# Performance work log

Measured on AMD Instinct MI355X. Metric: run time of the kernel, lower is better.

## Reference

```python
import jax, jax.numpy as jnp
import numpy as np

N_TREE = 200
DEPTH = 3
N_LEAF = 2 ** (DEPTH + 1) - 1      # 15 internal decision nodes
N_LEAVES = N_LEAF + 1              # 16 leaves
N_NODE = 64
BATCH = 2048
D_FEAT = 512
LR = 0.01


def _leaf_paths(depth):
    """For each of the 2^(depth+1) leaves, the internal-node index and the
    left/right bit at every level (matches the tf.gather index construction:
    bit==0 -> take p, bit==1 -> take 1-p; children of node n are 2n+1, 2n+2)."""
    L = 2 ** (depth + 1)
    nodes = np.zeros((L, depth + 1), np.int32)
    bits = np.zeros((L, depth + 1), np.int32)
    for l in range(L):
        node = 0
        for d in range(depth + 1):
            bit = (l >> (depth - d)) & 1
            nodes[l, d] = node
            bits[l, d] = bit
            node = 2 * node + 1 + bit
    return nodes, bits

_NODES, _BITS = _leaf_paths(DEPTH)


def setup_inputs() -> dict:
    key = jax.random.key(0)
    ks = jax.random.split(key, 9)
    u = lambda k, s: jax.random.uniform(k, s, jnp.float32, -0.05, 0.05)  # keras 'uniform' init
    return {
        "x": jax.random.normal(ks[0], (BATCH, D_FEAT), jnp.float32),
        "y_true": jax.random.normal(ks[1], (BATCH, 1), jnp.float32),
        "w_t": u(ks[2], (N_TREE, D_FEAT, N_NODE)),
        "b_t": u(ks[3], (N_TREE, N_NODE)),
        "w_d": u(ks[4], (N_TREE, N_NODE, N_LEAF)),
        "b_d": u(ks[5], (N_TREE, N_LEAF)),
        "w_l": u(ks[6], (N_TREE, N_LEAVES)),
        "b_l": u(ks[7], (N_TREE,)),
        "f_0": jnp.full((1,), 0.5, jnp.float32),
    }


def reference(x, y_true, w_t, b_t, w_d, b_d, w_l, b_l, f_0):
    B = x.shape[0]
    # Batched per-tree small MLP (the 200-iteration Python loop in the original).
    # Dropout is identity at inference.
    h = jax.nn.relu(jnp.einsum('bd,tdn->tbn', x, w_t) + b_t[:, None, :])        # [T,B,N_NODE]
    p = jax.nn.sigmoid(jnp.einsum('tbn,tnl->tbl', h, w_d) + b_d[:, None, :])    # [T,B,15]
    # Soft binary-tree routing: mu[t,b,leaf] = prod over path of p or (1-p).
    # This reproduces the tiled-index tf.gather construction exactly.
    pn = p[..., _NODES]                                                         # [T,B,16,DEPTH+1]
    q = jnp.where(_BITS == 1, 1.0 - pn, pn)
    mu = jnp.prod(q, axis=-1)                                                   # [T,B,16]
    # Per-tree leaf score with tanh.
    f = jnp.tanh(jnp.einsum('tbl,tl->tb', mu, w_l) + b_l[:, None])              # [T,B]
    # Sequential boosting accumulation: predict_k = f_0 + lr * sum_{i<k} f_i.
    cum = f_0 + LR * jnp.cumsum(f.T, axis=1)                                    # [B,T]
    py_x = jnp.concatenate([jnp.broadcast_to(f_0[None, :], (B, 1)), cum], axis=1)  # [B,T+1]
    return py_x
```

## Files before the change

kernel.cpp:

```cpp
#include <hip/hip_runtime.h>

#define T_TREES 200
#define BATCH   2048
#define D_FEAT  512
#define N_NODE  64
#define LR      0.01f

typedef __attribute__((__ext_vector_type__(8)))  __bf16 bf16x8;
typedef __attribute__((__ext_vector_type__(16))) float  f32x16;

__device__ __forceinline__ unsigned short f32_to_bf16(float f) {
    unsigned u = __float_as_uint(f);
    u += 0x7FFFu + ((u >> 16) & 1u);
    return (unsigned short)(u >> 16);
}

__device__ __forceinline__ void gload_lds16(const void* g, void* l) {
    __builtin_amdgcn_global_load_lds(
        (__attribute__((address_space(1))) void*)(void*)g,
        (__attribute__((address_space(3))) void*)l,
        16, 0, 0);
}

__global__ __launch_bounds__(256) void prep_all(
    const float* __restrict__ x, const float* __restrict__ w_t,
    const float* __restrict__ w_d,
    unsigned short* __restrict__ x_p, unsigned short* __restrict__ w_p,
    unsigned short* __restrict__ w_dt) {
    __shared__ float tile[64 * 65];
    int b = blockIdx.x;
    if (b < 256) {
        int mb = b >> 3, slab = b & 7;
        const float* src = x + (mb * 64) * D_FEAT + slab * 64;
        #pragma unroll
        for (int p = 0; p < 16; ++p) {
            int idx = p * 256 + threadIdx.x;
            int r = idx >> 6, c = idx & 63;
            tile[r * 65 + c] = src[r * D_FEAT + c];
        }
        __syncthreads();
        int mt = mb >> 1, mq = mb & 1;
        unsigned short* dst = x_p + mt * 65536 + slab * 8192 + mq * 512;
        #pragma unroll
        for (int p = 0; p < 2; ++p) {
            int sid = p * 256 + threadIdx.x;
            int kgl = sid >> 6;
            int r   = sid & 63;
            const float* sr = &tile[r * 65 + kgl * 8];
            bf16x8 o;
            #pragma unroll
            for (int j = 0; j < 8; ++j) o[j] = (__bf16)sr[j];
            *(bf16x8*)(dst + kgl * 1024 + r * 8) = o;
        }
    } else if (b < 1920) {
        int g  = b & 7;
        int j  = (b - 256) >> 3;
        int pj = j >> 4;
        int r8 = j & 15;
        int tq = r8 >> 3, slab = r8 & 7;
        int pair = g * 13 + pj;
        if (pair >= 100) return;
        int t = pair * 2 + tq;
        const float* src = w_t + t * (D_FEAT * N_NODE) + slab * 64 * N_NODE;
        #pragma unroll
        for (int p = 0; p < 16; ++p) {
            int idx = p * 256 + threadIdx.x;
            int d = idx >> 6, n = idx & 63;
            tile[d * 65 + n] = src[d * N_NODE + n];
        }
        __syncthreads();
        unsigned short* dst = w_p + pair * 65536 + slab * 8192 + tq * 512;
        #pragma unroll
        for (int p = 0; p < 2; ++p) {
            int sid = p * 256 + threadIdx.x;
            int kgl = sid >> 6;
            int n   = sid & 63;
            bf16x8 o;
            #pragma unroll
            for (int j2 = 0; j2 < 8; ++j2) o[j2] = (__bf16)tile[(kgl * 8 + j2) * 65 + n];
            *(bf16x8*)(dst + kgl * 1024 + n * 8) = o;
        }
    } else {
        int g = b & 7;
        int j = (b - 1920) >> 3;
        int t = g * 26 + (j >> 3);
        if (t >= 200) return;
        int sub = j & 7;
        int e = t * 2048 + sub * 256 + threadIdx.x;
        int n = e & 63;
        int l = (e >> 6) & 31;
        float v = (l < 15) ? w_d[(t * 64 + n) * 15 + l] : 0.f;
        w_dt[e] = f32_to_bf16(v);
    }
}

__global__ __launch_bounds__(256, 4) void gbdt_main(
    const unsigned short* __restrict__ x_p,
    const unsigned short* __restrict__ w_p,
    const unsigned short* __restrict__ w_dt,
    const float* __restrict__ b_t,
    const float* __restrict__ b_d,
    const float* __restrict__ w_l,
    const float* __restrict__ b_l,
    float* __restrict__ f_ws)
{
    __shared__ alignas(16) char smem[34816];
    unsigned short* Hs = (unsigned short*)smem;
    __bf16*         Hb = (__bf16*)smem;
    float*          Pf = (float*)smem;

    const int tid    = threadIdx.x;
    const int lane   = tid & 63;
    const int w      = tid >> 6;
    const int lane31 = lane & 31;
    const int kh     = lane >> 5;
    const int wm     = w >> 1;
    const int wn     = w & 1;

    const int xcd  = blockIdx.x & 7;
    const int slot = blockIdx.x >> 3;
    const int mt   = slot & 15;
    const int pj   = slot >> 4;
    const int pair = xcd * 13 + pj;
    if (pair >= 100) return;
    const int t0 = pair * 2;
    const int m0 = mt * 128;

    const unsigned short* pA = x_p + mt * 65536 + kh * 1024 + (wm * 64 + lane31) * 8;
    const char* gb = (const char*)(w_p + pair * 65536) + tid * 16;

    const int boff = kh * 2048 + (wn * 64 + lane31) * 16;

    f32x16 acc[2][2];
    #pragma unroll
    for (int mb = 0; mb < 2; ++mb)
        #pragma unroll
        for (int nb = 0; nb < 2; ++nb)
            acc[mb][nb] = (f32x16)(0.f);

#define LOAD_A(cn, areg) do {                                      \
        _Pragma("unroll")                                          \
        for (int s2 = 0; s2 < 2; ++s2)                             \
            _Pragma("unroll")                                      \
            for (int mb = 0; mb < 2; ++mb)                         \
                (areg)[s2 * 2 + mb] =                              \
                    *(const bf16x8*)(pA + (cn) * 4096 + s2 * 2048 + mb * 256); \
    } while (0)

#define STAGE_B(cn, base) do {                                            \
        gload_lds16(gb + (cn) * 8192,        (base) + tid * 16);          \
        gload_lds16(gb + (cn) * 8192 + 4096, (base) + tid * 16 + 4096);   \
    } while (0)

    bf16x8 aC[4], aN[4];
    LOAD_A(0, aC);
    STAGE_B(0, smem);
    STAGE_B(1, smem + 8192);

    char* rd  = smem;
    char* rd1 = smem + 8192;
    char* st2 = smem + 16384;

    #pragma unroll
    for (int c = 0; c < 16; ++c) {
        if (c < 15) asm volatile("s_waitcnt vmcnt(2)" ::: "memory");
        else        asm volatile("s_waitcnt vmcnt(0)" ::: "memory");
        __builtin_amdgcn_s_barrier();
        if (c < 15) LOAD_A(c + 1, aN);
        if (c < 14) STAGE_B(c + 2, st2);
        __builtin_amdgcn_s_setprio(1);
        #pragma unroll
        for (int s2 = 0; s2 < 2; ++s2) {
            bf16x8 bv0 = *(const bf16x8*)(rd + boff + s2 * 4096);
            bf16x8 bv1 = *(const bf16x8*)(rd + boff + s2 * 4096 + 512);
            acc[0][0] = __builtin_amdgcn_mfma_f32_32x32x16_bf16(aC[s2 * 2 + 0], bv0, acc[0][0], 0, 0, 0);
            acc[0][1] = __builtin_amdgcn_mfma_f32_32x32x16_bf16(aC[s2 * 2 + 0], bv1, acc[0][1], 0, 0, 0);
            acc[1][0] = __builtin_amdgcn_mfma_f32_32x32x16_bf16(aC[s2 * 2 + 1], bv0, acc[1][0], 0, 0, 0);
            acc[1][1] = __builtin_amdgcn_mfma_f32_32x32x16_bf16(aC[s2 * 2 + 1], bv1, acc[1][1], 0, 0, 0);
        }
        __builtin_amdgcn_s_setprio(0);
        char* t = rd; rd = rd1; rd1 = st2; st2 = t;
        #pragma unroll
        for (int i = 0; i < 4; ++i) aC[i] = aN[i];
    }

    __syncthreads();

    #pragma unroll
    for (int nb = 0; nb < 2; ++nb) {
        float btv = b_t[(t0 + wn) * 64 + nb * 32 + lane31];
        #pragma unroll
        for (int mb = 0; mb < 2; ++mb)
            #pragma unroll
            for (int r = 0; r < 16; ++r) {
                int m = wm * 64 + mb * 32 + (r & 3) + 8 * (r >> 2) + 4 * kh;
                float h = fmaxf(acc[mb][nb][r] + btv, 0.f);
                Hb[wn * 8704 + m * 68 + nb * 32 + lane31] = (__bf16)h;
            }
    }
    __syncthreads();

    f32x16 acc2[2] = { (f32x16)(0.f), (f32x16)(0.f) };
    const unsigned short* pW = w_dt + (t0 + wn) * 2048 + lane31 * 64 + kh * 8;
    __builtin_amdgcn_s_setprio(1);
    #pragma unroll
    for (int s = 0; s < 4; ++s) {
        bf16x8 bv = *(const bf16x8*)(pW + s * 16);
        #pragma unroll
        for (int i = 0; i < 2; ++i) {
            const unsigned short* pH =
                Hs + wn * 8704 + (wm * 64 + i * 32 + lane31) * 68 + s * 16 + kh * 8;
            bf16x8 av = *(const bf16x8*)pH;
            acc2[i] = __builtin_amdgcn_mfma_f32_32x32x16_bf16(av, bv, acc2[i], 0, 0, 0);
        }
    }
    __builtin_amdgcn_s_setprio(0);
    __syncthreads();

    if (lane31 < 15) {
        float bdv = b_d[(t0 + wn) * 15 + lane31];
        #pragma unroll
        for (int i = 0; i < 2; ++i)
            #pragma unroll
            for (int r = 0; r < 16; ++r) {
                int m = wm * 64 + i * 32 + (r & 3) + 8 * (r >> 2) + 4 * kh;
                float lg = acc2[i][r] + bdv;
                Pf[(wn * 128 + m) * 17 + lane31] = 1.f / (1.f + __expf(-lg));
            }
    }
    __syncthreads();

    {
        int m = tid & 127;
        int j = tid >> 7;
        int t = t0 + j;
        float pv[15];
        #pragma unroll
        for (int i = 0; i < 15; ++i) pv[i] = Pf[(j * 128 + m) * 17 + i];
        float facc = 0.f;
        #pragma unroll
        for (int leaf = 0; leaf < 16; ++leaf) {
            float mu = 1.f;
            int node = 0;
            #pragma unroll
            for (int d = 0; d < 4; ++d) {
                int bit = (leaf >> (3 - d)) & 1;
                float p = pv[node];
                mu *= bit ? (1.f - p) : p;
                node = 2 * node + 1 + bit;
            }
            facc += mu * w_l[t * 16 + leaf];
        }
        f_ws[(m0 + m) * T_TREES + t] = tanhf(facc + b_l[t]);
    }
#undef STAGE_B
#undef LOAD_A
}

__global__ __launch_bounds__(256) void scan_k(const float* __restrict__ f_ws,
                                              const float* __restrict__ f0p,
                                              float* __restrict__ out) {
    int lane = threadIdx.x & 63, wid = threadIdx.x >> 6;
    int b = blockIdx.x * 4 + wid;
    float f0 = f0p[0];
    float4 v;
    if (lane < 50) v = *(const float4*)(f_ws + b * T_TREES + lane * 4);
    else           v = make_float4(0.f, 0.f, 0.f, 0.f);
    float p0 = v.x;
    float p1 = p0 + v.y;
    float p2 = p1 + v.z;
    float p3 = p2 + v.w;
    float s = p3;
    #pragma unroll
    for (int off = 1; off < 64; off <<= 1) {
        float y = __shfl_up(s, off, 64);
        if (lane >= off) s += y;
    }
    float excl = s - p3;
    if (lane < 50) {
        float* o = out + b * (T_TREES + 1) + 1 + lane * 4;
        o[0] = f0 + LR * (excl + p0);
        o[1] = f0 + LR * (excl + p1);
        o[2] = f0 + LR * (excl + p2);
        o[3] = f0 + LR * (excl + p3);
    }
    if (lane == 0) out[b * (T_TREES + 1)] = f0;
}

extern "C" void kernel_launch(void* const* d_in, const int* in_sizes, int n_in,
                              void* d_out, int out_size, void* d_ws, size_t ws_size,
                              hipStream_t stream) {
    const float* x   = (const float*)d_in[0];
    const float* w_t = (const float*)d_in[2];
    const float* b_t = (const float*)d_in[3];
    const float* w_d = (const float*)d_in[4];
    const float* b_d = (const float*)d_in[5];
    const float* w_l = (const float*)d_in[6];
    const float* b_l = (const float*)d_in[7];
    const float* f_0 = (const float*)d_in[8];
    float* out = (float*)d_out;

    char* ws = (char*)d_ws;
    unsigned short* x_p  = (unsigned short*)(ws);
    unsigned short* w_p  = (unsigned short*)(ws + 2097152);
    unsigned short* w_dt = (unsigned short*)(ws + 15204352);
    float*          f_ws = (float*)(ws + 16023552);

    prep_all<<<3584, 256, 0, stream>>>(x, w_t, w_d, x_p, w_p, w_dt);
    gbdt_main<<<1664, 256, 0, stream>>>(x_p, w_p, w_dt, b_t, b_d, w_l, b_l, f_ws);
    scan_k<<<512, 256, 0, stream>>>(f_ws, f_0, out);
}
```

Baseline: 129.9 us.

## Switch main kernel to single-wave blocks with barrier-free double-buffered pipeline

Replaces the 4-wave 128-row tile with a single-wave 64-row x 128-col (two trees) tile, launching twice as many 64-thread blocks. Each wave now stages its own B tile via 8 LDS-direct loads per chunk into a 2-deep buffer, so all s_barrier/__syncthreads are replaced by waitcnt. The cost targeted is block-wide synchronisation and the tail of the epilogue phases. In exchange, B tiles are no longer shared across waves, so each wave issues more global loads per FLOP and LDS reuse drops.

```diff
diff --git a/kernel.cpp b/kernel.cpp
--- a/kernel.cpp
+++ b/kernel.cpp
@@ -94,7 +94,7 @@
     }
 }
 
-__global__ __launch_bounds__(256, 4) void gbdt_main(
+__global__ __launch_bounds__(64, 2) void gbdt_main(
     const unsigned short* __restrict__ x_p,
     const unsigned short* __restrict__ w_p,
     const unsigned short* __restrict__ w_dt,
@@ -104,38 +104,35 @@
     const float* __restrict__ b_l,
     float* __restrict__ f_ws)
 {
-    __shared__ alignas(16) char smem[34816];
+    __shared__ alignas(16) char smem[17408];
     unsigned short* Hs = (unsigned short*)smem;
     __bf16*         Hb = (__bf16*)smem;
     float*          Pf = (float*)smem;
 
     const int tid    = threadIdx.x;
-    const int lane   = tid & 63;
-    const int w      = tid >> 6;
-    const int lane31 = lane & 31;
-    const int kh     = lane >> 5;
-    const int wm     = w >> 1;
-    const int wn     = w & 1;
-
-    const int xcd  = blockIdx.x & 7;
-    const int slot = blockIdx.x >> 3;
-    const int mt   = slot & 15;
-    const int pj   = slot >> 4;
+    const int lane31 = tid & 31;
+    const int kh     = tid >> 5;
+
+    const int b    = blockIdx.x;
+    const int xcd  = b & 7;
+    const int s    = b >> 3;
+    const int jobm = s & 31;
+    const int pj   = s >> 5;
     const int pair = xcd * 13 + pj;
     if (pair >= 100) return;
-    const int t0 = pair * 2;
-    const int m0 = mt * 128;
-
-    const unsigned short* pA = x_p + mt * 65536 + kh * 1024 + (wm * 64 + lane31) * 8;
+    const int t0   = pair * 2;
+    const int mt   = jobm >> 1;
+    const int half = jobm & 1;
+
+    const unsigned short* pA =
+        x_p + mt * 65536 + kh * 1024 + half * 512 + lane31 * 8;
     const char* gb = (const char*)(w_p + pair * 65536) + tid * 16;
 
-    const int boff = kh * 2048 + (wn * 64 + lane31) * 16;
-
-    f32x16 acc[2][2];
+    f32x16 acc[2][4];
     #pragma unroll
     for (int mb = 0; mb < 2; ++mb)
         #pragma unroll
-        for (int nb = 0; nb < 2; ++nb)
+        for (int nb = 0; nb < 4; ++nb)
             acc[mb][nb] = (f32x16)(0.f);
 
 #define LOAD_A(cn, areg) do {                                      \
@@ -147,96 +144,106 @@
                     *(const bf16x8*)(pA + (cn) * 4096 + s2 * 2048 + mb * 256); \
     } while (0)
 
-#define STAGE_B(cn, base) do {                                            \
-        gload_lds16(gb + (cn) * 8192,        (base) + tid * 16);          \
-        gload_lds16(gb + (cn) * 8192 + 4096, (base) + tid * 16 + 4096);   \
+#define STAGE_B(cn, base) do {                                     \
+        _Pragma("unroll")                                          \
+        for (int k = 0; k < 8; ++k)                                \
+            gload_lds16(gb + (cn) * 8192 + k * 1024,               \
+                        (base) + tid * 16 + k * 1024);             \
     } while (0)
 
     bf16x8 aC[4], aN[4];
+    STAGE_B(0, smem);
     LOAD_A(0, aC);
-    STAGE_B(0, smem);
-    STAGE_B(1, smem + 8192);
-
-    char* rd  = smem;
-    char* rd1 = smem + 8192;
-    char* st2 = smem + 16384;
 
     #pragma unroll
     for (int c = 0; c < 16; ++c) {
-        if (c < 15) asm volatile("s_waitcnt vmcnt(2)" ::: "memory");
-        else        asm volatile("s_waitcnt vmcnt(0)" ::: "memory");
-        __builtin_amdgcn_s_barrier();
-        if (c < 15) LOAD_A(c + 1, aN);
-        if (c < 14) STAGE_B(c + 2, st2);
+        if (c < 15) {
+            STAGE_B(c + 1, smem + ((c + 1) & 1) * 8192);
+            LOAD_A(c + 1, aN);
+            asm volatile("s_waitcnt vmcnt(12)" ::: "memory");
+        } else {
+            asm volatile("s_waitcnt vmcnt(0)" ::: "memory");
+        }
+        const char* buf = smem + (c & 1) * 8192;
         __builtin_amdgcn_s_setprio(1);
         #pragma unroll
         for (int s2 = 0; s2 < 2; ++s2) {
-            bf16x8 bv0 = *(const bf16x8*)(rd + boff + s2 * 4096);
-            bf16x8 bv1 = *(const bf16x8*)(rd + boff + s2 * 4096 + 512);
-            acc[0][0] = __builtin_amdgcn_mfma_f32_32x32x16_bf16(aC[s2 * 2 + 0], bv0, acc[0][0], 0, 0, 0);
-            acc[0][1] = __builtin_amdgcn_mfma_f32_32x32x16_bf16(aC[s2 * 2 + 0], bv1, acc[0][1], 0, 0, 0);
-            acc[1][0] = __builtin_amdgcn_mfma_f32_32x32x16_bf16(aC[s2 * 2 + 1], bv0, acc[1][0], 0, 0, 0);
-            acc[1][1] = __builtin_amdgcn_mfma_f32_32x32x16_bf16(aC[s2 * 2 + 1], bv1, acc[1][1], 0, 0, 0);
+            const int kgl = 2 * s2 + kh;
+            bf16x8 bv[4];
+            #pragma unroll
+            for (int nb = 0; nb < 4; ++nb)
+                bv[nb] = *(const bf16x8*)(buf + (kgl * 128 + nb * 32 + lane31) * 16);
+            #pragma unroll
+            for (int mb = 0; mb < 2; ++mb)
+                #pragma unroll
+                for (int nb = 0; nb < 4; ++nb)
+                    acc[mb][nb] = __builtin_amdgcn_mfma_f32_32x32x16_bf16(
+                        aC[s2 * 2 + mb], bv[nb], acc[mb][nb], 0, 0, 0);
         }
         __builtin_amdgcn_s_setprio(0);
-        char* t = rd; rd = rd1; rd1 = st2; st2 = t;
         #pragma unroll
         for (int i = 0; i < 4; ++i) aC[i] = aN[i];
     }
 
-    __syncthreads();
-
-    #pragma unroll
-    for (int nb = 0; nb < 2; ++nb) {
-        float btv = b_t[(t0 + wn) * 64 + nb * 32 + lane31];
+    #pragma unroll
+    for (int nb = 0; nb < 4; ++nb) {
+        float btv = b_t[(t0 + (nb >> 1)) * 64 + (nb & 1) * 32 + lane31];
         #pragma unroll
         for (int mb = 0; mb < 2; ++mb)
             #pragma unroll
             for (int r = 0; r < 16; ++r) {
-                int m = wm * 64 + mb * 32 + (r & 3) + 8 * (r >> 2) + 4 * kh;
-                float h = fmaxf(acc[mb][nb][r] + btv, 0.f);
-                Hb[wn * 8704 + m * 68 + nb * 32 + lane31] = (__bf16)h;
+                int m = mb * 32 + (r & 3) + 8 * (r >> 2) + 4 * kh;
+                float hv = fmaxf(acc[mb][nb][r] + btv, 0.f);
+                Hb[m * 136 + nb * 32 + lane31] = (__bf16)hv;
             }
     }
-    __syncthreads();
-
-    f32x16 acc2[2] = { (f32x16)(0.f), (f32x16)(0.f) };
-    const unsigned short* pW = w_dt + (t0 + wn) * 2048 + lane31 * 64 + kh * 8;
-    __builtin_amdgcn_s_setprio(1);
-    #pragma unroll
-    for (int s = 0; s < 4; ++s) {
-        bf16x8 bv = *(const bf16x8*)(pW + s * 16);
-        #pragma unroll
-        for (int i = 0; i < 2; ++i) {
-            const unsigned short* pH =
-                Hs + wn * 8704 + (wm * 64 + i * 32 + lane31) * 68 + s * 16 + kh * 8;
-            bf16x8 av = *(const bf16x8*)pH;
-            acc2[i] = __builtin_amdgcn_mfma_f32_32x32x16_bf16(av, bv, acc2[i], 0, 0, 0);
-        }
-    }
-    __builtin_amdgcn_s_setprio(0);
-    __syncthreads();
+    asm volatile("s_waitcnt lgkmcnt(0)" ::: "memory");
+
+    f32x16 acc2[2][2];
+    #pragma unroll
+    for (int j = 0; j < 2; ++j)
+        #pragma unroll
+        for (int i = 0; i < 2; ++i)
+            acc2[j][i] = (f32x16)(0.f);
+    #pragma unroll
+    for (int j = 0; j < 2; ++j) {
+        const unsigned short* pW = w_dt + (t0 + j) * 2048 + lane31 * 64 + kh * 8;
+        #pragma unroll
+        for (int s4 = 0; s4 < 4; ++s4) {
+            bf16x8 bv = *(const bf16x8*)(pW + s4 * 16);
+            #pragma unroll
+            for (int i = 0; i < 2; ++i) {
+                bf16x8 av = *(const bf16x8*)(
+                    Hs + (i * 32 + lane31) * 136 + j * 64 + s4 * 16 + kh * 8);
+                acc2[j][i] = __builtin_amdgcn_mfma_f32_32x32x16_bf16(
+                    av, bv, acc2[j][i], 0, 0, 0);
+            }
+        }
+    }
+    asm volatile("s_waitcnt lgkmcnt(0)" ::: "memory");
 
     if (lane31 < 15) {
-        float bdv = b_d[(t0 + wn) * 15 + lane31];
-        #pragma unroll
-        for (int i = 0; i < 2; ++i)
-            #pragma unroll
-            for (int r = 0; r < 16; ++r) {
-                int m = wm * 64 + i * 32 + (r & 3) + 8 * (r >> 2) + 4 * kh;
-                float lg = acc2[i][r] + bdv;
-                Pf[(wn * 128 + m) * 17 + lane31] = 1.f / (1.f + __expf(-lg));
-            }
-    }
-    __syncthreads();
-
-    {
-        int m = tid & 127;
-        int j = tid >> 7;
-        int t = t0 + j;
+        #pragma unroll
+        for (int j = 0; j < 2; ++j) {
+            float bdv = b_d[(t0 + j) * 15 + lane31];
+            #pragma unroll
+            for (int i = 0; i < 2; ++i)
+                #pragma unroll
+                for (int r = 0; r < 16; ++r) {
+                    int m = i * 32 + (r & 3) + 8 * (r >> 2) + 4 * kh;
+                    float lg = acc2[j][i][r] + bdv;
+                    Pf[(j * 64 + m) * 17 + lane31] = 1.f / (1.f + __expf(-lg));
+                }
+        }
+    }
+    asm volatile("s_waitcnt lgkmcnt(0)" ::: "memory");
+
+    #pragma unroll
+    for (int jj = 0; jj < 2; ++jj) {
+        int t = t0 + jj;
         float pv[15];
         #pragma unroll
-        for (int i = 0; i < 15; ++i) pv[i] = Pf[(j * 128 + m) * 17 + i];
+        for (int i = 0; i < 15; ++i) pv[i] = Pf[(jj * 64 + tid) * 17 + i];
         float facc = 0.f;
         #pragma unroll
         for (int leaf = 0; leaf < 16; ++leaf) {
@@ -251,7 +258,7 @@
             }
             facc += mu * w_l[t * 16 + leaf];
         }
-        f_ws[(m0 + m) * T_TREES + t] = tanhf(facc + b_l[t]);
+        f_ws[(jobm * 64 + tid) * T_TREES + t] = tanhf(facc + b_l[t]);
     }
 #undef STAGE_B
 #undef LOAD_A
@@ -307,6 +314,6 @@
     float*          f_ws = (float*)(ws + 16023552);
 
     prep_all<<<3584, 256, 0, stream>>>(x, w_t, w_d, x_p, w_p, w_dt);
-    gbdt_main<<<1664, 256, 0, stream>>>(x_p, w_p, w_dt, b_t, b_d, w_l, b_l, f_ws);
+    gbdt_main<<<3328, 64, 0, stream>>>(x_p, w_p, w_dt, b_t, b_d, w_l, b_l, f_ws);
     scan_k<<<512, 256, 0, stream>>>(f_ws, f_0, out);
 }
```

After: 140.0 us. +7.7%, slower.
